# Optimization experiments

Measured on AMD Instinct MI355X. Metric: run time of the kernel, lower is better.

Reference implementation:

```python
import jax, jax.numpy as jnp
import numpy as np

K = 3  # neighbors for knn_interpolate


def _knn_interpolate(x, pos, pos_skip, B, k):
    """PyG knn_interpolate with equal-sized batches.
    x: [N_coarse, C], pos: [N_coarse, 3], pos_skip: [N_fine, 3].
    """
    C = x.shape[1]
    xb = x.reshape(B, -1, C)          # [B, nc, C]
    pb = pos.reshape(B, -1, 3)        # [B, nc, 3]
    qb = pos_skip.reshape(B, -1, 3)   # [B, nf, 3]

    def per_cloud(xf, pf, qf):
        # squared distances [nf, nc]
        d2 = jnp.sum((qf[:, None, :] - pf[None, :, :]) ** 2, axis=-1)
        neg_d2k, idx = jax.lax.top_k(-d2, k)          # k smallest distances
        d2k = -neg_d2k                                # [nf, k]
        w = 1.0 / jnp.clip(d2k, 1e-16)                # inverse-distance weights
        w = jax.lax.stop_gradient(w)                  # PyG computes weights under no_grad
        feats = xf[idx]                               # [nf, k, C] gather
        return jnp.sum(w[..., None] * feats, axis=1) / jnp.sum(w, axis=1, keepdims=True)

    y = jax.vmap(per_cloud)(xb, pb, qb)               # [B, nf, C]
    return y.reshape(-1, C)


def setup_inputs() -> dict:
    key = jax.random.key(0)
    ks = jax.random.split(key, 8)
    B, n_coarse, n_fine = 16, 1024, 4096
    C_in, C_skip, C_mid, C_out = 256, 128, 256, 256
    x = jax.random.normal(ks[0], (B * n_coarse, C_in), jnp.float32)
    pos = jax.random.uniform(ks[1], (B * n_coarse, 3), jnp.float32)
    x_skip = jax.random.normal(ks[2], (B * n_fine, C_skip), jnp.float32)
    pos_skip = jax.random.uniform(ks[3], (B * n_fine, 3), jnp.float32)
    batch = jnp.repeat(jnp.arange(B, dtype=jnp.int64), n_coarse)
    batch_skip = jnp.repeat(jnp.arange(B, dtype=jnp.int64), n_fine)
    seed_idx = jnp.arange(B * n_coarse, dtype=jnp.int64)
    seed_idx_skip = jnp.arange(B * n_fine, dtype=jnp.int64)
    W1 = jax.random.normal(ks[4], (C_in + C_skip, C_mid), jnp.float32) * 0.05
    b1 = jnp.zeros((C_mid,), jnp.float32)
    W2 = jax.random.normal(ks[5], (C_mid, C_out), jnp.float32) * 0.05
    b2 = jnp.zeros((C_out,), jnp.float32)
    return {"x": x, "pos": pos, "batch": batch, "seed_idx": seed_idx,
            "x_skip": x_skip, "pos_skip": pos_skip, "batch_skip": batch_skip,
            "seed_idx_skip": seed_idx_skip, "W1": W1, "b1": b1, "W2": W2, "b2": b2}


def reference(x, pos, batch, seed_idx, x_skip, pos_skip, batch_skip, seed_idx_skip,
              W1, b1, W2, b2):
    B = int(batch[-1]) + 1  # equal-sized contiguous clouds
    y = _knn_interpolate(x, pos, pos_skip, B, K)      # [N_fine, C_in]
    h = jnp.concatenate([y, x_skip], axis=1)          # [N_fine, C_in+C_skip]
    h = jax.nn.relu(h @ W1 + b1)                      # MLP layer 1
    out = jax.nn.relu(h @ W2 + b2)                    # MLP layer 2
    return (out, pos_skip, batch_skip)
```

## Files before the change

kernel.cpp:

```cpp
#include <hip/hip_runtime.h>
#include <hip/hip_bf16.h>

#define NB    16
#define NC    1024
#define NF    4096
#define NFINE (NB*NF)
#define CIN   256
#define CSKIP 128
#define KH    (CIN+CSKIP)
#define CMID  256
#define COUT  256

typedef __attribute__((ext_vector_type(8))) short short8;
typedef __attribute__((ext_vector_type(4))) float f32x4;
typedef __attribute__((ext_vector_type(4))) unsigned int u32x4;

__device__ __forceinline__ float bf2f(short s) {
    return __uint_as_float(((unsigned)(unsigned short)s) << 16);
}

__global__ __launch_bounds__(256)
void binprep_kernel(const float* __restrict__ pos,
                    float* __restrict__ gp, int* __restrict__ gcs,
                    const float* __restrict__ W1, const float* __restrict__ W2,
                    __hip_bfloat16* __restrict__ W1at,
                    __hip_bfloat16* __restrict__ W1bt,
                    __hip_bfloat16* __restrict__ W2t)
{
    __shared__ int cnt[512];
    __shared__ float lx[NC], ly[NC], lz[NC];
    __shared__ short lcell[NC];
    const int t = threadIdx.x;
    if (blockIdx.x >= NB) {
        int e = (blockIdx.x - NB)*256 + t;
        if (e < CMID*CIN) {
            int n = e / CIN, k = e % CIN;
            W1at[e] = __float2bfloat16(W1[(size_t)k*CMID + n]);
        }
        int e2 = e - CMID*CIN;
        if (e2 >= 0 && e2 < CMID*CSKIP) {
            int n = e2 / CSKIP, k = e2 % CSKIP;
            W1bt[e2] = __float2bfloat16(W1[(size_t)(CIN + k)*CMID + n]);
        }
        int e3 = e - CMID*CIN - CMID*CSKIP;
        if (e3 >= 0 && e3 < COUT*CMID) {
            int n = e3 / CMID, k = e3 % CMID;
            W2t[e3] = __float2bfloat16(W2[(size_t)k*COUT + n]);
        }
        return;
    }
    const int b = blockIdx.x;
    for (int i = t; i < 512; i += 256) cnt[i] = 0;
    __syncthreads();
    const float* pc = pos + (size_t)b*NC*3;
    #pragma unroll
    for (int u = 0; u < 4; ++u) {
        int i = t + u*256;
        float x = pc[3*i+0], y = pc[3*i+1], z = pc[3*i+2];
        int cx = min(7, (int)(x*8.0f));
        int cy = min(7, (int)(y*8.0f));
        int cz = min(7, (int)(z*8.0f));
        int c = (cz*8 + cy)*8 + cx;
        lx[i] = x; ly[i] = y; lz[i] = z; lcell[i] = (short)c;
        atomicAdd(&cnt[c], 1);
    }
    __syncthreads();
    if (t < 64) {
        int v[8]; int s = 0;
        #pragma unroll
        for (int u = 0; u < 8; ++u) { v[u] = cnt[t*8+u]; s += v[u]; }
        int pfx = s;
        #pragma unroll
        for (int m = 1; m < 64; m <<= 1) {
            int o = __shfl_up(pfx, m);
            if (t >= m) pfx += o;
        }
        pfx -= s;
        #pragma unroll
        for (int u = 0; u < 8; ++u) {
            gcs[b*513 + t*8+u] = pfx;
            cnt[t*8+u] = pfx;
            pfx += v[u];
        }
        if (t == 63) gcs[b*513 + 512] = NC;
    }
    __syncthreads();
    #pragma unroll
    for (int u = 0; u < 4; ++u) {
        int i = t + u*256;
        int c = lcell[i];
        int dst = atomicAdd(&cnt[c], 1);
        f32x4 v; v[0] = lx[i]; v[1] = ly[i]; v[2] = lz[i]; v[3] = __int_as_float(i);
        *(f32x4*)&gp[(size_t)(b*NC + dst)*4] = v;
    }
}

#define KQPB 64

#define INS(d, j) do {                                        \
    bool c2 = (d) < dB, c1 = (d) < dA, c0 = (d) < d0;         \
    dB = c1 ? dA : (c2 ? (d) : dB);                           \
    iB = c1 ? iA : (c2 ? (j) : iB);                           \
    dA = c0 ? d0 : (c1 ? (d) : dA);                           \
    iA = c0 ? i0 : (c1 ? (j) : iA);                           \
    d0 = c0 ? (d) : d0;                                       \
    i0 = c0 ? (j) : i0;                                       \
} while (0)

#define SCAN(JS, JE) for (int j = (JS) + g; j < (JE); j += 8) {        \
    const f32x4 p = *(const f32x4*)&pp[j][0];                          \
    float fx = qx - p[0], fy = qy - p[1], fz = qz - p[2];              \
    float dd = fx*fx + fy*fy + fz*fz;                                  \
    INS(dd, j);                                                        \
}

#define MERGE8() do {                                                          \
    _Pragma("unroll")                                                          \
    for (int mm = 1; mm < 8; mm <<= 1) {                                       \
        float e0 = __shfl_xor(d0, mm), e1 = __shfl_xor(dA, mm), e2 = __shfl_xor(dB, mm); \
        int   f0 = __shfl_xor(i0, mm), f1 = __shfl_xor(iA, mm), f2 = __shfl_xor(iB, mm); \
        INS(e0, f0); INS(e1, f1); INS(e2, f2);                                 \
    }                                                                          \
} while (0)

union KZMem {
    struct { float pp[NC][4]; unsigned short cs[513]; } k;
    struct { short As[64][64]; short Bs[256][64]; } z;
};

__global__ __launch_bounds__(512, 2)
void knnZ_kernel(const float* __restrict__ pos_skip,
                 const float* __restrict__ gp,
                 const int* __restrict__ gcs,
                 int* __restrict__ widx, float* __restrict__ wval,
                 float* __restrict__ out,
                 const float* __restrict__ x,
                 const __hip_bfloat16* __restrict__ W1at,
                 __hip_bfloat16* __restrict__ Z)
{
    __shared__ __align__(16) KZMem sm;
    const int t = threadIdx.x;

    if (blockIdx.x >= 1024) {
        const int m0 = (blockIdx.x - 1024) * 64;
        const int wave = t >> 6, lane = t & 63;
        const int wm = wave >> 2, wn = wave & 3;
        const int rl = lane & 15, kq = lane >> 4;
        const short* Br = (const short*)W1at;
        const int ar = t >> 3;
        const int ac = t & 7;
        f32x4 rA[2];
        u32x4 rB[4];

        #define LOADAZ(K0) do {                                                \
            const float* p = &x[(size_t)(m0+ar)*CIN + (K0) + ac*8];            \
            rA[0] = *(const f32x4*)p; rA[1] = *(const f32x4*)(p+4);            \
        } while (0)
        #define LOADBZ(K0) do {                                                \
            _Pragma("unroll")                                                  \
            for (int i = 0; i < 4; ++i) {                                      \
                const int ch = t + i*512;                                      \
                const int rr = ch >> 3, cc = ch & 7;                           \
                rB[i] = *(const u32x4*)&Br[(size_t)rr*CIN + (K0) + cc*8];      \
            }                                                                  \
        } while (0)

        f32x4 acc[2][4] = {};
        LOADAZ(0); LOADBZ(0);
        #pragma unroll
        for (int s = 0; s < 4; ++s) {
            __syncthreads();
            {
                short8 sv;
                #pragma unroll
                for (int u = 0; u < 2; ++u) {
                    f32x4 a = rA[u];
                    #pragma unroll
                    for (int e = 0; e < 4; ++e) {
                        __hip_bfloat16 bb = __float2bfloat16(a[e]);
                        ((short*)&sv)[u*4+e] = *(short*)&bb;
                    }
                }
                *(short8*)&sm.z.As[ar][(ac ^ (ar&7))*8] = sv;
            }
            #pragma unroll
            for (int i = 0; i < 4; ++i) {
                const int ch = t + i*512;
                const int rr = ch >> 3, cc = ch & 7;
                *(u32x4*)&sm.z.Bs[rr][(cc ^ (rr&7))*8] = rB[i];
            }
            __syncthreads();
            if (s < 3) { LOADAZ((s+1)*64); LOADBZ((s+1)*64); }
            #pragma unroll
            for (int kh = 0; kh < 2; ++kh) {
                const int kc = kh*4 + kq;
                short8 af[2], bf[4];
                #pragma unroll
                for (int mf = 0; mf < 2; ++mf)
                    af[mf] = *(const short8*)&sm.z.As[wm*32 + mf*16 + rl][(kc ^ (rl&7))*8];
                #pragma unroll
                for (int nf = 0; nf < 4; ++nf)
                    bf[nf] = *(const short8*)&sm.z.Bs[wn*64 + nf*16 + rl][(kc ^ (rl&7))*8];
                #pragma unroll
                for (int mf = 0; mf < 2; ++mf)
                #pragma unroll
                for (int nf = 0; nf < 4; ++nf)
                    acc[mf][nf] = __builtin_amdgcn_mfma_f32_16x16x32_bf16(af[mf], bf[nf], acc[mf][nf], 0,0,0);
            }
        }
        #undef LOADAZ
        #undef LOADBZ
        #pragma unroll
        for (int mf = 0; mf < 2; ++mf)
        #pragma unroll
        for (int nf = 0; nf < 4; ++nf) {
            const int col = wn*64 + nf*16 + rl;
            #pragma unroll
            for (int i = 0; i < 4; ++i) {
                const int row = m0 + wm*32 + mf*16 + kq*4 + i;
                Z[(size_t)row*CMID + col] = __float2bfloat16(acc[mf][nf][i]);
            }
        }
        return;
    }

    float (*pp)[4] = sm.k.pp;
    unsigned short* cs = sm.k.cs;
    const int bpc = NF/KQPB;
    const int b  = blockIdx.x / bpc;
    const int qb = blockIdx.x % bpc;

    {
        int e = blockIdx.x*192 + t;
        if (t < 192) out[(size_t)NFINE*COUT + e] = pos_skip[e];
        if (t >= 192 && t < 256) {
            int e2 = blockIdx.x*64 + (t - 192);
            out[(size_t)NFINE*COUT + (size_t)NFINE*3 + e2] = (float)(e2 >> 12);
        }
    }

    for (int i = t; i < NC; i += 512)
        *(f32x4*)&pp[i][0] = *(const f32x4*)&gp[(size_t)(b*NC + i)*4];
    for (int i = t; i < 513; i += 512) cs[i] = (unsigned short)gcs[b*513 + i];
    __syncthreads();

    const int g  = t & 7;
    const int ql = t >> 3;
    const int q  = b*NF + qb*KQPB + ql;
    const float qx = pos_skip[(size_t)q*3+0];
    const float qy = pos_skip[(size_t)q*3+1];
    const float qz = pos_skip[(size_t)q*3+2];
    const int cx = min(7, (int)(qx*8.0f));
    const int cy = min(7, (int)(qy*8.0f));
    const int cz = min(7, (int)(qz*8.0f));

    float d0 = 3.0e38f, dA = 3.0e38f, dB = 3.0e38f;
    int   i0 = 0,       iA = 0,       iB = 0;

    const int xlo = max(cx-1,0), xhi = min(cx+1,7);
    const int ylo = max(cy-1,0), yhi = min(cy+1,7);
    const int zlo = max(cz-1,0), zhi = min(cz+1,7);
    #pragma unroll
    for (int r = 0; r < 9; ++r) {
        const int z = cz - 1 + r/3;
        const int y = cy - 1 + r%3;
        const bool ok = ((unsigned)z < 8u) & ((unsigned)y < 8u);
        const int rb = (z*8 + y)*8;
        int js = 0, je = 0;
        if (ok) { js = cs[rb + xlo]; je = cs[rb + xhi + 1]; }
        SCAN(js, je);
    }
    MERGE8();

    float m1 = 3.0e38f;
    if (xlo > 0) m1 = fminf(m1, qx - xlo*0.125f);
    if (xhi < 7) m1 = fminf(m1, (xhi+1)*0.125f - qx);
    if (ylo > 0) m1 = fminf(m1, qy - ylo*0.125f);
    if (yhi < 7) m1 = fminf(m1, (yhi+1)*0.125f - qy);
    if (zlo > 0) m1 = fminf(m1, qz - zlo*0.125f);
    if (zhi < 7) m1 = fminf(m1, (zhi+1)*0.125f - qz);

    if (dB > m1*m1) {
        const float s0 = d0, s1 = dA, s2 = dB;
        const int   t0 = i0, t1 = iA, t2 = iB;
        d0 = dA = dB = 3.0e38f; i0 = iA = iB = 0;
        const int xlo2 = max(cx-2,0), xhi2 = min(cx+2,7);
        const int ylo2 = max(cy-2,0), yhi2 = min(cy+2,7);
        const int zlo2 = max(cz-2,0), zhi2 = min(cz+2,7);
        for (int z = zlo2; z <= zhi2; ++z)
        for (int y = ylo2; y <= yhi2; ++y) {
            const int rb = (z*8 + y)*8;
            const bool inner_zy = (z >= zlo && z <= zhi && y >= ylo && y <= yhi);
            int jsA, jeA, jsB, jeB;
            if (inner_zy) {
                jsA = cs[rb + xlo2]; jeA = cs[rb + xlo];
                jsB = cs[rb + xhi + 1]; jeB = cs[rb + xhi2 + 1];
            } else {
                jsA = cs[rb + xlo2]; jeA = cs[rb + xhi2 + 1];
                jsB = 0; jeB = 0;
            }
            SCAN(jsA, jeA);
            SCAN(jsB, jeB);
        }
        MERGE8();
        INS(s0, t0); INS(s1, t1); INS(s2, t2);

        float m2 = 3.0e38f;
        if (xlo2 > 0) m2 = fminf(m2, qx - xlo2*0.125f);
        if (xhi2 < 7) m2 = fminf(m2, (xhi2+1)*0.125f - qx);
        if (ylo2 > 0) m2 = fminf(m2, qy - ylo2*0.125f);
        if (yhi2 < 7) m2 = fminf(m2, (yhi2+1)*0.125f - qy);
        if (zlo2 > 0) m2 = fminf(m2, qz - zlo2*0.125f);
        if (zhi2 < 7) m2 = fminf(m2, (zhi2+1)*0.125f - qz);
        if (dB > m2*m2) {
            const float u0 = d0, u1 = dA, u2 = dB;
            const int   v0 = i0, v1 = iA, v2 = iB;
            d0 = dA = dB = 3.0e38f; i0 = iA = iB = 0;
            for (int j = g; j < NC; j += 8) {
                const f32x4 p = *(const f32x4*)&pp[j][0];
                int pcx = min(7, (int)(p[0]*8.0f));
                int pcy = min(7, (int)(p[1]*8.0f));
                int pcz = min(7, (int)(p[2]*8.0f));
                if (pcx >= xlo2 && pcx <= xhi2 && pcy >= ylo2 && pcy <= yhi2 &&
                    pcz >= zlo2 && pcz <= zhi2) continue;
                float fx = qx - p[0], fy = qy - p[1], fz = qz - p[2];
                float dd = fx*fx + fy*fy + fz*fz;
                INS(dd, j);
            }
            MERGE8();
            INS(u0, v0); INS(u1, v1); INS(u2, v2);
        }
    }

    if (g == 0) {
        const int o0 = __float_as_int(pp[i0][3]);
        const int o1 = __float_as_int(pp[iA][3]);
        const int o2 = __float_as_int(pp[iB][3]);
        float w0 = 1.0f / fmaxf(d0, 1e-16f);
        float w1 = 1.0f / fmaxf(dA, 1e-16f);
        float w2 = 1.0f / fmaxf(dB, 1e-16f);
        float inv = 1.0f / (w0 + w1 + w2);
        widx[q*3+0] = b*NC + o0;  wval[q*3+0] = w0*inv;
        widx[q*3+1] = b*NC + o1;  wval[q*3+1] = w1*inv;
        widx[q*3+2] = b*NC + o2;  wval[q*3+2] = w2*inv;
    }
}

#define SLOTA(c, r)  (((c) & 8) | (((c) & 7) ^ ((r) & 7)))
#define SLOTB(c, r)  ((c) ^ ((r) & 3))
#define SLOTH(c, r)  (((c) & 24) | (((c) & 7) ^ ((r) & 7)))

__global__ __launch_bounds__(512, 8)
void g2f32_kernel(const float* __restrict__ x_skip,
                  const __hip_bfloat16* __restrict__ W1bt,
                  const float* __restrict__ b1,
                  const __hip_bfloat16* __restrict__ Z,
                  const int* __restrict__ widx,
                  const float* __restrict__ wval,
                  const __hip_bfloat16* __restrict__ W2t,
                  const float* __restrict__ b2,
                  float* __restrict__ out)
{
    __shared__ __align__(16) short As[32][128];
    __shared__ __align__(16) short Bs[256][32];
    __shared__ __align__(16) short Hs[32][256];
    const int nwg = gridDim.x;
    const int tile = (blockIdx.x & 7)*(nwg >> 3) + (blockIdx.x >> 3);
    const int m0 = tile * 32;

    const int t = threadIdx.x;
    const int wn = t >> 6;
    const int lane = t & 63;
    const int rl = lane & 15, kq = lane >> 4;
    const short* Bg  = (const short*)W1bt;
    const short* B2r = (const short*)W2t;
    const short* Zr  = (const short*)Z;

    {
        const int ar = t >> 4, ac = t & 15;
        const float* xs = &x_skip[(size_t)(m0+ar)*CSKIP + ac*8];
        f32x4 a0 = *(const f32x4*)xs;
        f32x4 a1 = *(const f32x4*)(xs+4);
        short8 sv;
        #pragma unroll
        for (int e = 0; e < 4; ++e) {
            __hip_bfloat16 ba = __float2bfloat16(a0[e]);
            __hip_bfloat16 bb = __float2bfloat16(a1[e]);
            ((short*)&sv)[e]   = *(short*)&ba;
            ((short*)&sv)[4+e] = *(short*)&bb;
        }
        *(short8*)&As[ar][SLOTA(ac,ar)*8] = sv;
    }

    const int brr = t >> 1, bcc = (t & 1)*2;
    short8 rB0, rB1;
    #define LOADBG(S) do {                                                     \
        const short* p = &Bg[(size_t)brr*CSKIP + (S)*32 + bcc*8];              \
        rB0 = *(const short8*)p; rB1 = *(const short8*)(p+8);                  \
    } while (0)
    #define LOADB2(S) do {                                                     \
        const short* p = &B2r[(size_t)brr*CMID + (S)*32 + bcc*8];              \
        rB0 = *(const short8*)p; rB1 = *(const short8*)(p+8);                  \
    } while (0)
    #define STAGEB() do {                                                      \
        *(short8*)&Bs[brr][SLOTB(bcc,brr)*8]   = rB0;                          \
        *(short8*)&Bs[brr][SLOTB(bcc+1,brr)*8] = rB1;                          \
    } while (0)

    f32x4 acc[2][2] = {};
    #define MFMAG(S) do {                                                      \
        const int kc = (S)*4 + kq;                                             \
        short8 af[2], bf[2];                                                   \
        af[0] = *(const short8*)&As[     rl][SLOTA(kc,rl)*8];                  \
        af[1] = *(const short8*)&As[16 + rl][SLOTA(kc,rl)*8];                  \
        bf[0] = *(const short8*)&Bs[wn*32 +      rl][SLOTB(kq,rl)*8];          \
        bf[1] = *(const short8*)&Bs[wn*32 + 16 + rl][SLOTB(kq,rl)*8];          \
        _Pragma("unroll")                                                      \
        for (int mf = 0; mf < 2; ++mf)                                         \
        _Pragma("unroll")                                                      \
        for (int nf = 0; nf < 2; ++nf)                                         \
            acc[mf][nf] = __builtin_amdgcn_mfma_f32_16x16x32_bf16(af[mf], bf[nf], acc[mf][nf], 0,0,0); \
    } while (0)

    LOADBG(0);
    STAGEB();
    __syncthreads();
    LOADBG(1);
    MFMAG(0);
    __syncthreads();
    STAGEB();
    __syncthreads();
    LOADBG(2);
    MFMAG(1);
    __syncthreads();
    STAGEB();
    __syncthreads();
    LOADBG(3);
    MFMAG(2);
    __syncthreads();
    STAGEB();
    __syncthreads();
    LOADB2(0);
    MFMAG(3);

    #pragma unroll
    for (int nf = 0; nf < 2; ++nf) {
        const int col = wn*32 + nf*16 + rl;
        const float bv = b1[col];
        const int cc = col >> 3;
        #pragma unroll
        for (int mf = 0; mf < 2; ++mf)
        #pragma unroll
        for (int i = 0; i < 4; ++i) {
            const int row = mf*16 + kq*4 + i;
            float v = acc[mf][nf][i] + bv;
            __hip_bfloat16 bb = __float2bfloat16(v);
            Hs[row][SLOTH(cc,row)*8 + (col & 7)] = *(short*)&bb;
        }
    }
    __syncthreads();
    STAGEB();

    #pragma unroll
    for (int u = 0; u < 2; ++u) {
        const int ch = t + u*512;
        const int row = ch >> 5;
        const int cc  = ch & 31;
        const int gr = (m0 + row)*3;
        const int j0 = widx[gr+0], j1 = widx[gr+1], j2 = widx[gr+2];
        const float w0 = wval[gr+0], w1 = wval[gr+1], w2 = wval[gr+2];
        const short8 z0 = *(const short8*)&Zr[(size_t)j0*CMID + cc*8];
        const short8 z1 = *(const short8*)&Zr[(size_t)j1*CMID + cc*8];
        const short8 z2 = *(const short8*)&Zr[(size_t)j2*CMID + cc*8];
        const int slot = SLOTH(cc,row)*8;
        short8 gchunk = *(const short8*)&Hs[row][slot];
        short8 r;
        #pragma unroll
        for (int e = 0; e < 8; ++e) {
            float v = bf2f(gchunk[e]) + w0*bf2f(z0[e]) + w1*bf2f(z1[e]) + w2*bf2f(z2[e]);
            v = fmaxf(v, 0.0f);
            __hip_bfloat16 bb = __float2bfloat16(v);
            r[e] = *(short*)&bb;
        }
        *(short8*)&Hs[row][slot] = r;
    }
    __syncthreads();

    f32x4 acc2[2][2] = {};
    #define MFMA2(S) do {                                                      \
        const int kca = (S)*4 + kq;                                            \
        short8 af[2], bf[2];                                                   \
        af[0] = *(const short8*)&Hs[     rl][SLOTH(kca,rl)*8];                 \
        af[1] = *(const short8*)&Hs[16 + rl][SLOTH(kca,rl)*8];                 \
        bf[0] = *(const short8*)&Bs[wn*32 +      rl][SLOTB(kq,rl)*8];          \
        bf[1] = *(const short8*)&Bs[wn*32 + 16 + rl][SLOTB(kq,rl)*8];          \
        _Pragma("unroll")                                                      \
        for (int mf = 0; mf < 2; ++mf)                                         \
        _Pragma("unroll")                                                      \
        for (int nf = 0; nf < 2; ++nf)                                         \
            acc2[mf][nf] = __builtin_amdgcn_mfma_f32_16x16x32_bf16(af[mf], bf[nf], acc2[mf][nf], 0,0,0); \
    } while (0)

    LOADB2(1); MFMA2(0); __syncthreads(); STAGEB(); __syncthreads();
    LOADB2(2); MFMA2(1); __syncthreads(); STAGEB(); __syncthreads();
    LOADB2(3); MFMA2(2); __syncthreads(); STAGEB(); __syncthreads();
    LOADB2(4); MFMA2(3); __syncthreads(); STAGEB(); __syncthreads();
    LOADB2(5); MFMA2(4); __syncthreads(); STAGEB(); __syncthreads();
    LOADB2(6); MFMA2(5); __syncthreads(); STAGEB(); __syncthreads();
    LOADB2(7); MFMA2(6); __syncthreads(); STAGEB(); __syncthreads();
    MFMA2(7);

    #pragma unroll
    for (int nf = 0; nf < 2; ++nf) {
        const int col = wn*32 + nf*16 + rl;
        const float bv = b2[col];
        #pragma unroll
        for (int mf = 0; mf < 2; ++mf)
        #pragma unroll
        for (int i = 0; i < 4; ++i) {
            const int row = m0 + mf*16 + kq*4 + i;
            out[(size_t)row*COUT + col] = fmaxf(acc2[mf][nf][i] + bv, 0.0f);
        }
    }
    #undef LOADBG
    #undef LOADB2
    #undef STAGEB
    #undef MFMAG
    #undef MFMA2
}

extern "C" void kernel_launch(void* const* d_in, const int* in_sizes, int n_in,
                              void* d_out, int out_size, void* d_ws, size_t ws_size,
                              hipStream_t stream) {
    const float* x        = (const float*)d_in[0];
    const float* pos      = (const float*)d_in[1];
    const float* x_skip   = (const float*)d_in[4];
    const float* pos_skip = (const float*)d_in[5];
    const float* W1       = (const float*)d_in[8];
    const float* b1       = (const float*)d_in[9];
    const float* W2       = (const float*)d_in[10];
    const float* b2       = (const float*)d_in[11];
    float* out = (float*)d_out;
    char* ws = (char*)d_ws;

    int*            widx = (int*)  (ws + 0);
    float*          wval = (float*)(ws + 786432);
    __hip_bfloat16* W1at = (__hip_bfloat16*)(ws + 1572864);
    __hip_bfloat16* W1bt = (__hip_bfloat16*)(ws + 1703936);
    __hip_bfloat16* W2t  = (__hip_bfloat16*)(ws + 1769472);
    float*          gp   = (float*)(ws + 1900544);
    int*            gcs  = (int*)  (ws + 2162688);
    __hip_bfloat16* Z    = (__hip_bfloat16*)(ws + 2195520);

    hipLaunchKernelGGL(binprep_kernel, dim3(NB + 640), dim3(256), 0, stream,
                       pos, gp, gcs, W1, W2, W1at, W1bt, W2t);
    hipLaunchKernelGGL(knnZ_kernel, dim3(1024 + 256), dim3(512), 0, stream,
                       pos_skip, gp, gcs, widx, wval, out, x, W1at, Z);
    hipLaunchKernelGGL(g2f32_kernel, dim3(NFINE/32), dim3(512), 0, stream,
                       x_skip, W1bt, b1, Z, widx, wval, W2t, b2, out);
}
```

Measured before the change: 73.44 us.

## Enlarge fused MLP tile to 64 rows with 2x4 wave grid and shared LDS

Rewrites the fused gather+MLP kernel to handle 64 rows per workgroup instead of 32, arranging the 8 waves as a 2x4 grid so each wave computes a 32x64 output block. The first-layer weight is staged in 64-wide K chunks, which halves the number of barrier-separated stages. The A, B and H tiles now share one aliased LDS buffer. The goal is to amortise the weight loads over twice as many rows and raise MFMA work per barrier, at the cost of more registers, fewer resident blocks, and half as many workgroups.

```diff
diff --git a/kernel.cpp b/kernel.cpp
--- a/kernel.cpp
+++ b/kernel.cpp
@@ -346,123 +346,143 @@
     }
 }
 
-#define SLOTA(c, r)  (((c) & 8) | (((c) & 7) ^ ((r) & 7)))
-#define SLOTB(c, r)  ((c) ^ ((r) & 3))
-#define SLOTH(c, r)  (((c) & 24) | (((c) & 7) ^ ((r) & 7)))
-
-__global__ __launch_bounds__(512, 8)
-void g2f32_kernel(const float* __restrict__ x_skip,
-                  const __hip_bfloat16* __restrict__ W1bt,
-                  const float* __restrict__ b1,
-                  const __hip_bfloat16* __restrict__ Z,
-                  const int* __restrict__ widx,
-                  const float* __restrict__ wval,
-                  const __hip_bfloat16* __restrict__ W2t,
-                  const float* __restrict__ b2,
-                  float* __restrict__ out)
+__global__ __launch_bounds__(512, 6)
+void g2v4_kernel(const float* __restrict__ x_skip,
+                 const __hip_bfloat16* __restrict__ W1bt,
+                 const float* __restrict__ b1,
+                 const __hip_bfloat16* __restrict__ Z,
+                 const int* __restrict__ widx,
+                 const float* __restrict__ wval,
+                 const __hip_bfloat16* __restrict__ W2t,
+                 const float* __restrict__ b2,
+                 float* __restrict__ out)
 {
-    __shared__ __align__(16) short As[32][128];
-    __shared__ __align__(16) short Bs[256][32];
-    __shared__ __align__(16) short Hs[32][256];
+    __shared__ __align__(16) short SM[24576];
+    short (*As)[128] = (short(*)[128])&SM[0];
+    short (*BsG)[64] = (short(*)[64]) &SM[8192];
+    short (*Bs2)[32] = (short(*)[32]) &SM[16384];
+
     const int nwg = gridDim.x;
     const int tile = (blockIdx.x & 7)*(nwg >> 3) + (blockIdx.x >> 3);
-    const int m0 = tile * 32;
+    const int m0 = tile * 64;
 
     const int t = threadIdx.x;
-    const int wn = t >> 6;
-    const int lane = t & 63;
+    const int wave = t >> 6, lane = t & 63;
+    const int wm = wave >> 2, wn = wave & 3;
     const int rl = lane & 15, kq = lane >> 4;
     const short* Bg  = (const short*)W1bt;
     const short* B2r = (const short*)W2t;
     const short* Zr  = (const short*)Z;
 
+    const int ar = t >> 3;
+    const int ac = t & 7;
+
+    const float* xs = &x_skip[(size_t)(m0+ar)*CSKIP];
+    f32x4 pa0 = *(const f32x4*)&xs[ac*8];
+    f32x4 pa1 = *(const f32x4*)&xs[ac*8+4];
+    f32x4 pb0 = *(const f32x4*)&xs[64+ac*8];
+    f32x4 pb1 = *(const f32x4*)&xs[64+ac*8+4];
+
+    u32x4 rG[4];
+    #define LOADBG(S) do {                                                     \
+        _Pragma("unroll")                                                      \
+        for (int i = 0; i < 4; ++i) {                                          \
+            const int ch = t + i*512;                                          \
+            const int rr = ch >> 3, cc = ch & 7;                               \
+            rG[i] = *(const u32x4*)&Bg[(size_t)rr*CSKIP + (S)*64 + cc*8];      \
+        }                                                                      \
+    } while (0)
+    #define STAGEBG() do {                                                     \
+        _Pragma("unroll")                                                      \
+        for (int i = 0; i < 4; ++i) {                                          \
+            const int ch = t + i*512;                                          \
+            const int rr = ch >> 3, cc = ch & 7;                               \
+            *(u32x4*)&BsG[rr][(cc ^ (rr&7))*8] = rG[i];                        \
+        }                                                                      \
+    } while (0)
+
+    short8 r20, r21;
+    #define LOADB2(S) do {                                                     \
+        const short* p = &B2r[(size_t)(t>>1)*CMID + (S)*32 + (t&1)*16];        \
+        r20 = *(const short8*)p; r21 = *(const short8*)(p+8);                  \
+    } while (0)
+    #define STAGEB2() do {                                                     \
+        const int rw = t >> 1, c0 = (t&1)*2, gg = (rw>>1)&3;                   \
+        *(short8*)&Bs2[rw][(c0 ^ gg)*8]     = r20;                             \
+        *(short8*)&Bs2[rw][((c0+1) ^ gg)*8] = r21;                             \
+    } while (0)
+
     {
-        const int ar = t >> 4, ac = t & 15;
-        const float* xs = &x_skip[(size_t)(m0+ar)*CSKIP + ac*8];
-        f32x4 a0 = *(const f32x4*)xs;
-        f32x4 a1 = *(const f32x4*)(xs+4);
-        short8 sv;
-        #pragma unroll
-        for (int e = 0; e < 4; ++e) {
-            __hip_bfloat16 ba = __float2bfloat16(a0[e]);
-            __hip_bfloat16 bb = __float2bfloat16(a1[e]);
-            ((short*)&sv)[e]   = *(short*)&ba;
-            ((short*)&sv)[4+e] = *(short*)&bb;
-        }
-        *(short8*)&As[ar][SLOTA(ac,ar)*8] = sv;
-    }
-
-    const int brr = t >> 1, bcc = (t & 1)*2;
-    short8 rB0, rB1;
-    #define LOADBG(S) do {                                                     \
-        const short* p = &Bg[(size_t)brr*CSKIP + (S)*32 + bcc*8];              \
-        rB0 = *(const short8*)p; rB1 = *(const short8*)(p+8);                  \
+        short8 sv0, sv1;
+        #pragma unroll
+        for (int u = 0; u < 2; ++u) {
+            f32x4 a = (u == 0) ? pa0 : pa1;
+            f32x4 b = (u == 0) ? pb0 : pb1;
+            #pragma unroll
+            for (int e = 0; e < 4; ++e) {
+                __hip_bfloat16 ba = __float2bfloat16(a[e]);
+                __hip_bfloat16 bb = __float2bfloat16(b[e]);
+                ((short*)&sv0)[u*4+e] = *(short*)&ba;
+                ((short*)&sv1)[u*4+e] = *(short*)&bb;
+            }
+        }
+        const int sw = ac ^ (ar & 7);
+        *(short8*)&As[ar][sw*8]     = sv0;
+        *(short8*)&As[ar][(8+sw)*8] = sv1;
+    }
+
+    f32x4 acc[2][4] = {};
+    #define MFMAG(S) do {                                                      \
+        _Pragma("unroll")                                                      \
+        for (int kh = 0; kh < 2; ++kh) {                                       \
+            const int kc = kh*4 + kq;                                          \
+            short8 af[2], bf[4];                                               \
+            _Pragma("unroll")                                                  \
+            for (int mf = 0; mf < 2; ++mf)                                     \
+                af[mf] = *(const short8*)&As[wm*32 + mf*16 + rl][((S)*8 + (kc ^ (rl&7)))*8]; \
+            _Pragma("unroll")                                                  \
+            for (int nf = 0; nf < 4; ++nf)                                     \
+                bf[nf] = *(const short8*)&BsG[wn*64 + nf*16 + rl][(kc ^ (rl&7))*8]; \
+            _Pragma("unroll")                                                  \
+            for (int mf = 0; mf < 2; ++mf)                                     \
+            _Pragma("unroll")                                                  \
+            for (int nf = 0; nf < 4; ++nf)                                     \
+                acc[mf][nf] = __builtin_amdgcn_mfma_f32_16x16x32_bf16(af[mf], bf[nf], acc[mf][nf], 0,0,0); \
+        }                                                                      \
     } while (0)
-    #define LOADB2(S) do {                                                     \
-        const short* p = &B2r[(size_t)brr*CMID + (S)*32 + bcc*8];              \
-        rB0 = *(const short8*)p; rB1 = *(const short8*)(p+8);                  \
-    } while (0)
-    #define STAGEB() do {                                                      \
-        *(short8*)&Bs[brr][SLOTB(bcc,brr)*8]   = rB0;                          \
-        *(short8*)&Bs[brr][SLOTB(bcc+1,brr)*8] = rB1;                          \
-    } while (0)
-
-    f32x4 acc[2][2] = {};
-    #define MFMAG(S) do {                                                      \
-        const int kc = (S)*4 + kq;                                             \
-        short8 af[2], bf[2];                                                   \
-        af[0] = *(const short8*)&As[     rl][SLOTA(kc,rl)*8];                  \
-        af[1] = *(const short8*)&As[16 + rl][SLOTA(kc,rl)*8];                  \
-        bf[0] = *(const short8*)&Bs[wn*32 +      rl][SLOTB(kq,rl)*8];          \
-        bf[1] = *(const short8*)&Bs[wn*32 + 16 + rl][SLOTB(kq,rl)*8];          \
-        _Pragma("unroll")                                                      \
-        for (int mf = 0; mf < 2; ++mf)                                         \
-        _Pragma("unroll")                                                      \
-        for (int nf = 0; nf < 2; ++nf)                                         \
-            acc[mf][nf] = __builtin_amdgcn_mfma_f32_16x16x32_bf16(af[mf], bf[nf], acc[mf][nf], 0,0,0); \
-    } while (0)
 
     LOADBG(0);
-    STAGEB();
+    STAGEBG();
     __syncthreads();
     LOADBG(1);
     MFMAG(0);
     __syncthreads();
-    STAGEB();
-    __syncthreads();
-    LOADBG(2);
+    STAGEBG();
+    __syncthreads();
+    LOADB2(0);
     MFMAG(1);
     __syncthreads();
-    STAGEB();
-    __syncthreads();
-    LOADBG(3);
-    MFMAG(2);
-    __syncthreads();
-    STAGEB();
-    __syncthreads();
-    LOADB2(0);
-    MFMAG(3);
-
-    #pragma unroll
-    for (int nf = 0; nf < 2; ++nf) {
-        const int col = wn*32 + nf*16 + rl;
+
+    #pragma unroll
+    for (int mf = 0; mf < 2; ++mf)
+    #pragma unroll
+    for (int nf = 0; nf < 4; ++nf) {
+        const int col = wn*64 + nf*16 + rl;
         const float bv = b1[col];
-        const int cc = col >> 3;
-        #pragma unroll
-        for (int mf = 0; mf < 2; ++mf)
+        short* hbase = &SM[wm*8192];
         #pragma unroll
         for (int i = 0; i < 4; ++i) {
-            const int row = mf*16 + kq*4 + i;
+            const int rlow = mf*16 + kq*4 + i;
             float v = acc[mf][nf][i] + bv;
             __hip_bfloat16 bb = __float2bfloat16(v);
-            Hs[row][SLOTH(cc,row)*8 + (col & 7)] = *(short*)&bb;
-        }
-    }
-    __syncthreads();
-    STAGEB();
-
-    #pragma unroll
-    for (int u = 0; u < 2; ++u) {
+            hbase[rlow*256 + ((col >> 3) ^ (rlow & 7))*8 + (col & 7)] = *(short*)&bb;
+        }
+    }
+    STAGEB2();
+    __syncthreads();
+
+    #pragma unroll
+    for (int u = 0; u < 4; ++u) {
         const int ch = t + u*512;
         const int row = ch >> 5;
         const int cc  = ch & 31;
@@ -472,8 +492,8 @@
         const short8 z0 = *(const short8*)&Zr[(size_t)j0*CMID + cc*8];
         const short8 z1 = *(const short8*)&Zr[(size_t)j1*CMID + cc*8];
         const short8 z2 = *(const short8*)&Zr[(size_t)j2*CMID + cc*8];
-        const int slot = SLOTH(cc,row)*8;
-        short8 gchunk = *(const short8*)&Hs[row][slot];
+        short* hp = &SM[(row & 31)*256 + (row >> 5)*8192 + ((cc ^ (row & 7)))*8];
+        short8 gchunk = *(const short8*)hp;
         short8 r;
         #pragma unroll
         for (int e = 0; e < 8; ++e) {
@@ -482,49 +502,64 @@
             __hip_bfloat16 bb = __float2bfloat16(v);
             r[e] = *(short*)&bb;
         }
-        *(short8*)&Hs[row][slot] = r;
-    }
-    __syncthreads();
-
-    f32x4 acc2[2][2] = {};
-    #define MFMA2(S) do {                                                      \
-        const int kca = (S)*4 + kq;                                            \
-        short8 af[2], bf[2];                                                   \
-        af[0] = *(const short8*)&Hs[     rl][SLOTH(kca,rl)*8];                 \
-        af[1] = *(const short8*)&Hs[16 + rl][SLOTH(kca,rl)*8];                 \
-        bf[0] = *(const short8*)&Bs[wn*32 +      rl][SLOTB(kq,rl)*8];          \
-        bf[1] = *(const short8*)&Bs[wn*32 + 16 + rl][SLOTB(kq,rl)*8];          \
+        *(short8*)hp = r;
+    }
+    LOADB2(1);
+    __syncthreads();
+
+    f32x4 acc2[2][4] = {};
+    #define MFMA2(S2) do {                                                     \
+        const int kca = (S2)*4 + kq;                                           \
+        short8 af[2], bf[4];                                                   \
+        _Pragma("unroll")                                                      \
+        for (int mf = 0; mf < 2; ++mf) {                                       \
+            const int rlow = mf*16 + rl;                                       \
+            af[mf] = *(const short8*)&SM[wm*8192 + rlow*256 + ((kca ^ (rlow & 7)))*8]; \
+        }                                                                      \
+        _Pragma("unroll")                                                      \
+        for (int nf = 0; nf < 4; ++nf) {                                       \
+            const int r2 = wn*64 + nf*16 + rl;                                 \
+            bf[nf] = *(const short8*)&Bs2[r2][(kq ^ ((r2>>1)&3))*8];           \
+        }                                                                      \
         _Pragma("unroll")                                                      \
         for (int mf = 0; mf < 2; ++mf)                                         \
         _Pragma("unroll")                                                      \
-        for (int nf = 0; nf < 2; ++nf)                                         \
+        for (int nf = 0; nf < 4; ++nf)                                         \
             acc2[mf][nf] = __builtin_amdgcn_mfma_f32_16x16x32_bf16(af[mf], bf[nf], acc2[mf][nf], 0,0,0); \
     } while (0)
 
-    LOADB2(1); MFMA2(0); __syncthreads(); STAGEB(); __syncthreads();
-    LOADB2(2); MFMA2(1); __syncthreads(); STAGEB(); __syncthreads();
-    LOADB2(3); MFMA2(2); __syncthreads(); STAGEB(); __syncthreads();
-    LOADB2(4); MFMA2(3); __syncthreads(); STAGEB(); __syncthreads();
-    LOADB2(5); MFMA2(4); __syncthreads(); STAGEB(); __syncthreads();
-    LOADB2(6); MFMA2(5); __syncthreads(); STAGEB(); __syncthreads();
-    LOADB2(7); MFMA2(6); __syncthreads(); STAGEB(); __syncthreads();
+    MFMA2(0);
+    __syncthreads(); STAGEB2(); __syncthreads(); LOADB2(2);
+    MFMA2(1);
+    __syncthreads(); STAGEB2(); __syncthreads(); LOADB2(3);
+    MFMA2(2);
+    __syncthreads(); STAGEB2(); __syncthreads(); LOADB2(4);
+    MFMA2(3);
+    __syncthreads(); STAGEB2(); __syncthreads(); LOADB2(5);
+    MFMA2(4);
+    __syncthreads(); STAGEB2(); __syncthreads(); LOADB2(6);
+    MFMA2(5);
+    __syncthreads(); STAGEB2(); __syncthreads(); LOADB2(7);
+    MFMA2(6);
+    __syncthreads(); STAGEB2(); __syncthreads();
     MFMA2(7);
 
     #pragma unroll
-    for (int nf = 0; nf < 2; ++nf) {
-        const int col = wn*32 + nf*16 + rl;
+    for (int mf = 0; mf < 2; ++mf)
+    #pragma unroll
+    for (int nf = 0; nf < 4; ++nf) {
+        const int col = wn*64 + nf*16 + rl;
         const float bv = b2[col];
         #pragma unroll
-        for (int mf = 0; mf < 2; ++mf)
-        #pragma unroll
         for (int i = 0; i < 4; ++i) {
-            const int row = m0 + mf*16 + kq*4 + i;
+            const int row = m0 + wm*32 + mf*16 + kq*4 + i;
             out[(size_t)row*COUT + col] = fmaxf(acc2[mf][nf][i] + bv, 0.0f);
         }
     }
     #undef LOADBG
+    #undef STAGEBG
     #undef LOADB2
-    #undef STAGEB
+    #undef STAGEB2
     #undef MFMAG
     #undef MFMA2
 }
@@ -556,6 +591,6 @@
                        pos, gp, gcs, W1, W2, W1at, W1bt, W2t);
     hipLaunchKernelGGL(knnZ_kernel, dim3(1024 + 256), dim3(512), 0, stream,
                        pos_skip, gp, gcs, widx, wval, out, x, W1at, Z);
-    hipLaunchKernelGGL(g2f32_kernel, dim3(NFINE/32), dim3(512), 0, stream,
+    hipLaunchKernelGGL(g2v4_kernel, dim3(NFINE/64), dim3(512), 0, stream,
                        x_skip, W1bt, b1, Z, widx, wval, W2t, b2, out);
 }
```

Measured after the change: 69.02 us. 6.0% less time.
